# Kernel tuning notes

Hardware: AMD Instinct MI355X
Metric: run time of the kernel (lower is better)

## Reference

```python
import jax, jax.numpy as jnp
import numpy as np

B, S, HID = 4, 1024, 1024
NH, HD = 16, 64  # num heads, head dim


def setup_inputs() -> dict:
    key = jax.random.key(0)
    ks = jax.random.split(key, 8)
    scale = 0.02
    return {
        "hidden_states": jax.random.normal(ks[0], (B, S, HID), dtype=jnp.float32),
        "attention_mask": jnp.ones((B, 1, 1, S), dtype=jnp.float32),
        "Wq": jax.random.normal(ks[1], (HID, HID), dtype=jnp.float32) * scale,
        "bq": jnp.zeros((HID,), dtype=jnp.float32),
        "Wk": jax.random.normal(ks[2], (HID, HID), dtype=jnp.float32) * scale,
        "bk": jnp.zeros((HID,), dtype=jnp.float32),
        "Wv": jax.random.normal(ks[3], (HID, HID), dtype=jnp.float32) * scale,
        "bv": jnp.zeros((HID,), dtype=jnp.float32),
    }


def reference(hidden_states, attention_mask, Wq, bq, Wk, bk, Wv, bv):
    # Linear projections: torch nn.Linear computes x @ W.T + b
    q = hidden_states @ Wq.T + bq  # [B,S,HID]
    k = hidden_states @ Wk.T + bk
    v = hidden_states @ Wv.T + bv

    def split_heads(x):
        return x.reshape(B, S, NH, HD).transpose(0, 2, 1, 3)  # [B,NH,S,HD]

    q, k, v = split_heads(q), split_heads(k), split_heads(v)

    scores = jnp.einsum("bhqd,bhkd->bhqk", q, k) / jnp.sqrt(jnp.float32(HD))
    # faithful to original: scores - (2 - mask) * 1e6
    scores = scores - (2.0 - attention_mask) * 1.0e6
    probs = jax.nn.softmax(scores, axis=-1)
    # dropout: eval mode -> identity
    ctx = jnp.einsum("bhqk,bhkd->bhqd", probs, v)  # [B,NH,S,HD]
    ctx = ctx.transpose(0, 2, 1, 3).reshape(B, S, HID)
    return ctx
```

## Files before the change

### kernel.cpp

```cpp
#include <hip/hip_runtime.h>
#include <math.h>

#define B_ 4
#define S_ 1024
#define HID_ 1024
#define NH_ 16
#define HD_ 64
#define NTOK (B_ * S_)

typedef __attribute__((ext_vector_type(4))) float f32x4;
typedef __attribute__((ext_vector_type(8))) short bf16x8;

__device__ __forceinline__ unsigned short f2bf(float f) {
    union { float f; unsigned int u; } v; v.f = f;
    unsigned int r = v.u + 0x7fffu + ((v.u >> 16) & 1u);
    return (unsigned short)(r >> 16);
}
__device__ __forceinline__ float bf2f(unsigned short u) {
    return __uint_as_float((unsigned int)u << 16);
}

__device__ __forceinline__ void load_lds16(const void* g, void* l) {
    __builtin_amdgcn_global_load_lds(
        (const __attribute__((address_space(1))) unsigned int*)(uintptr_t)g,
        (__attribute__((address_space(3))) unsigned int*)(uintptr_t)l,
        16, 0, 0);
}

__global__ __launch_bounds__(256) void cvt_all(
    const float* __restrict__ x, const float* __restrict__ wq,
    const float* __restrict__ wk, const float* __restrict__ wv,
    unsigned short* __restrict__ xb, unsigned short* __restrict__ wqb,
    unsigned short* __restrict__ wkb, unsigned short* __restrict__ wvb)
{
    const int which = blockIdx.y;
    const float* src = which == 0 ? x : which == 1 ? wq : which == 2 ? wk : wv;
    unsigned short* dst = which == 0 ? xb : which == 1 ? wqb : which == 2 ? wkb : wvb;
    const int n4 = (which == 0) ? (NTOK * HID_ / 4) : (HID_ * HID_ / 4);
    int i = blockIdx.x * 256 + threadIdx.x;
    if (i < n4) {
        float4 f = ((const float4*)src)[i];
        ushort4 o = make_ushort4(f2bf(f.x), f2bf(f.y), f2bf(f.z), f2bf(f.w));
        ((ushort4*)dst)[i] = o;
    }
}

__global__ __launch_bounds__(256) void qkv_gemm_mfma(
    const unsigned short* __restrict__ xb,
    const unsigned short* __restrict__ Wqb, const float* __restrict__ bq,
    const unsigned short* __restrict__ Wkb, const float* __restrict__ bk,
    const unsigned short* __restrict__ Wvb, const float* __restrict__ bv,
    unsigned short* __restrict__ qout, unsigned short* __restrict__ kout,
    unsigned short* __restrict__ vtout)
{
    const int which = blockIdx.z;
    const unsigned short* __restrict__ W = which == 0 ? Wqb : which == 1 ? Wkb : Wvb;
    const float* __restrict__ bias       = which == 0 ? bq  : which == 1 ? bk  : bv;

    __shared__ unsigned short As[128 * 64];
    __shared__ unsigned short Bs[128 * 64];

    const int t    = threadIdx.x;
    const int lane = t & 63;
    const int w    = t >> 6;
    const int wr   = w >> 1;
    const int wc   = w & 1;
    const int g    = lane >> 4;
    const int lrow = lane & 15;

    const int bm = blockIdx.x;
    const int bn = blockIdx.y;

    const unsigned short* __restrict__ Arow = (which == 2) ? W  : xb;
    const unsigned short* __restrict__ Brow = (which == 2) ? xb : W;
    const int am0 = (which == 2) ? bn * 128 : bm * 128;
    const int bn0 = (which == 2) ? bm * 128 : bn * 128;

    const int srow = t >> 3;
    const int sc   = ((t & 7) ^ ((t >> 3) & 7)) << 3;
    const unsigned short* gA = Arow + (size_t)(am0 + srow) * HID_ + sc;
    const unsigned short* gB = Brow + (size_t)(bn0 + srow) * HID_ + sc;

    const f32x4 zero = {0.f, 0.f, 0.f, 0.f};
    f32x4 acc[4][4];
    #pragma unroll
    for (int i = 0; i < 4; ++i)
        #pragma unroll
        for (int j = 0; j < 4; ++j) acc[i][j] = zero;

    for (int k0 = 0; k0 < HID_; k0 += 64) {
        __syncthreads();
        #pragma unroll
        for (int i = 0; i < 4; ++i) {
            load_lds16(gA + (size_t)(i * 32) * HID_ + k0, (char*)As + i * 4096 + t * 16);
            load_lds16(gB + (size_t)(i * 32) * HID_ + k0, (char*)Bs + i * 4096 + t * 16);
        }
        __syncthreads();

        #pragma unroll
        for (int ks = 0; ks < 2; ++ks) {
            bf16x8 af[4], bf[4];
            #pragma unroll
            for (int i = 0; i < 4; ++i) {
                const int row = wr * 64 + i * 16 + lrow;
                af[i] = *(const bf16x8*)&As[row * 64 + (((ks * 4 + g) ^ (row & 7)) << 3)];
            }
            #pragma unroll
            for (int j = 0; j < 4; ++j) {
                const int row = wc * 64 + j * 16 + lrow;
                bf[j] = *(const bf16x8*)&Bs[row * 64 + (((ks * 4 + g) ^ (row & 7)) << 3)];
            }
            #pragma unroll
            for (int i = 0; i < 4; ++i)
                #pragma unroll
                for (int j = 0; j < 4; ++j)
                    acc[i][j] = __builtin_amdgcn_mfma_f32_16x16x32_bf16(
                        af[i], bf[j], acc[i][j], 0, 0, 0);
        }
    }

    const int col   = lane & 15;
    const int rbase = (lane >> 4) << 2;
    if (which == 2) {
        #pragma unroll
        for (int i = 0; i < 4; ++i) {
            #pragma unroll
            for (int r = 0; r < 4; ++r) {
                const int feat = bn * 128 + wr * 64 + i * 16 + rbase + r;
                const int h = feat >> 6, d = feat & 63;
                const float bias_v = bias[feat];
                #pragma unroll
                for (int j = 0; j < 4; ++j) {
                    const int tok = bm * 128 + wc * 64 + j * 16 + col;
                    const int b = tok >> 10, s = tok & 1023;
                    vtout[((size_t)((b << 4) + h) << 16) + ((size_t)d << 10) + s] =
                        f2bf(acc[i][j][r] + bias_v);
                }
            }
        }
    } else {
        #pragma unroll
        for (int j = 0; j < 4; ++j) {
            const int feat = bn * 128 + wc * 64 + j * 16 + col;
            const int h = feat >> 6, d = feat & 63;
            const float bias_v = bias[feat];
            #pragma unroll
            for (int i = 0; i < 4; ++i) {
                const int tok0 = bm * 128 + wr * 64 + i * 16 + rbase;
                #pragma unroll
                for (int r = 0; r < 4; ++r) {
                    const int tok = tok0 + r;
                    const int b = tok >> 10, s = tok & 1023;
                    const size_t off = ((size_t)((b << 4) + h) << 16) + ((size_t)s << 6) + d;
                    const float val = acc[i][j][r] + bias_v;
                    if (which == 0) qout[off] = f2bf(val);
                    else            kout[off] = f2bf(val);
                }
            }
        }
    }
}

__global__ __launch_bounds__(256) void attn_mfma(
    const unsigned short* __restrict__ Q, const unsigned short* __restrict__ K,
    const unsigned short* __restrict__ Vt, const float* __restrict__ mask,
    float* __restrict__ out)
{
    __shared__ unsigned short Qs[64 * 64];
    __shared__ unsigned short Ks[64 * 64];
    __shared__ unsigned short Vts[64 * 64];
    __shared__ unsigned short Ps[4][16 * 72];
    __shared__ float Ls[4][16];
    __shared__ float Ms[64];

    const int t    = threadIdx.x;
    const int lane = t & 63;
    const int w    = t >> 6;
    const int g    = lane >> 4;
    const int ln   = lane & 15;

    const int bh = blockIdx.x;
    const int b  = bh >> 4;
    const int h  = bh & 15;
    const int q0 = blockIdx.y << 6;

    const unsigned short* __restrict__ qg = Q  + ((size_t)bh << 16);
    const unsigned short* __restrict__ kg = K  + ((size_t)bh << 16);
    const unsigned short* __restrict__ vg = Vt + ((size_t)bh << 16);

    #pragma unroll
    for (int i = 0; i < 2; ++i) {
        const int G   = i * 256 + t;
        const int row = G >> 3;
        const int c   = (G & 7) ^ (row & 7);
        load_lds16(qg + (size_t)(q0 + row) * 64 + c * 8, (char*)Qs + i * 4096 + t * 16);
    }

    const f32x4 zero = {0.f, 0.f, 0.f, 0.f};
    f32x4 O[4];
    #pragma unroll
    for (int j = 0; j < 4; ++j) O[j] = zero;
    float lacc = 0.f;

    const int qrow = w * 16 + ln;

    for (int kt = 0; kt < 16; ++kt) {
        const int kt0 = kt << 6;
        __syncthreads();
        #pragma unroll
        for (int i = 0; i < 2; ++i) {
            const int G   = i * 256 + t;
            const int row = G >> 3;
            const int c   = (G & 7) ^ (row & 7);
            load_lds16(kg + (size_t)(kt0 + row) * 64 + c * 8, (char*)Ks  + i * 4096 + t * 16);
            load_lds16(vg + (size_t)row * 1024 + kt0 + c * 8, (char*)Vts + i * 4096 + t * 16);
        }
        if (t < 64) Ms[t] = mask[(b << 10) + kt0 + t];
        __syncthreads();

        f32x4 sacc[4];
        #pragma unroll
        for (int j = 0; j < 4; ++j) sacc[j] = zero;
        #pragma unroll
        for (int ks = 0; ks < 2; ++ks) {
            bf16x8 qf = *(const bf16x8*)&Qs[qrow * 64 + (((ks * 4 + g) ^ (qrow & 7)) << 3)];
            bf16x8 kf[4];
            #pragma unroll
            for (int j = 0; j < 4; ++j) {
                const int krow = j * 16 + ln;
                kf[j] = *(const bf16x8*)&Ks[krow * 64 + (((ks * 4 + g) ^ (krow & 7)) << 3)];
            }
            #pragma unroll
            for (int j = 0; j < 4; ++j)
                sacc[j] = __builtin_amdgcn_mfma_f32_16x16x32_bf16(
                    kf[j], qf, sacc[j], 0, 0, 0);
        }

        #pragma unroll
        for (int j = 0; j < 4; ++j) {
            unsigned short pb[4];
            #pragma unroll
            for (int r = 0; r < 4; ++r) {
                const int key = j * 16 + g * 4 + r;
                const float sv = sacc[j][r] * 0.125f - (2.0f - Ms[key]) * 1.0e6f;
                pb[r] = f2bf(__expf(sv + 1.0e6f));
                lacc += bf2f(pb[r]);
            }
            uint2 pk;
            pk.x = (unsigned int)pb[0] | ((unsigned int)pb[1] << 16);
            pk.y = (unsigned int)pb[2] | ((unsigned int)pb[3] << 16);
            *(uint2*)&Ps[w][ln * 72 + j * 16 + (g << 2)] = pk;
        }
        asm volatile("s_waitcnt lgkmcnt(0)" ::: "memory");

        #pragma unroll
        for (int ks = 0; ks < 2; ++ks) {
            bf16x8 pf = *(const bf16x8*)&Ps[w][ln * 72 + ks * 32 + (g << 3)];
            bf16x8 vf[4];
            #pragma unroll
            for (int j = 0; j < 4; ++j) {
                const int vrow = j * 16 + ln;
                vf[j] = *(const bf16x8*)&Vts[vrow * 64 + (((ks * 4 + g) ^ (vrow & 7)) << 3)];
            }
            #pragma unroll
            for (int j = 0; j < 4; ++j)
                O[j] = __builtin_amdgcn_mfma_f32_16x16x32_bf16(
                    pf, vf[j], O[j], 0, 0, 0);
        }
    }

    float rs = lacc;
    rs += __shfl_xor(rs, 16);
    rs += __shfl_xor(rs, 32);
    if (lane < 16) Ls[w][ln] = rs;
    asm volatile("s_waitcnt lgkmcnt(0)" ::: "memory");
    #pragma unroll
    for (int r = 0; r < 4; ++r) {
        const float inv = 1.0f / Ls[w][(g << 2) + r];
        const int q = q0 + w * 16 + (g << 2) + r;
        const size_t base = (((size_t)(b << 10) + q) << 10) + (h << 6);
        #pragma unroll
        for (int j = 0; j < 4; ++j)
            out[base + j * 16 + ln] = O[j][r] * inv;
    }
}

extern "C" void kernel_launch(void* const* d_in, const int* in_sizes, int n_in,
                              void* d_out, int out_size, void* d_ws, size_t ws_size,
                              hipStream_t stream) {
    const float* hs   = (const float*)d_in[0];
    const float* mask = (const float*)d_in[1];
    const float* Wq   = (const float*)d_in[2];
    const float* bq   = (const float*)d_in[3];
    const float* Wk   = (const float*)d_in[4];
    const float* bk   = (const float*)d_in[5];
    const float* Wv   = (const float*)d_in[6];
    const float* bv   = (const float*)d_in[7];
    float* out = (float*)d_out;

    char* ws = (char*)d_ws;
    unsigned short* xb  = (unsigned short*)(ws);
    unsigned short* wqb = (unsigned short*)(ws + ((size_t)8  << 20));
    unsigned short* wkb = (unsigned short*)(ws + ((size_t)10 << 20));
    unsigned short* wvb = (unsigned short*)(ws + ((size_t)12 << 20));
    unsigned short* qb  = (unsigned short*)(ws + ((size_t)14 << 20));
    unsigned short* kb  = (unsigned short*)(ws + ((size_t)22 << 20));
    unsigned short* vtb = (unsigned short*)(ws + ((size_t)30 << 20));

    cvt_all<<<dim3(4096, 4), 256, 0, stream>>>(hs, Wq, Wk, Wv, xb, wqb, wkb, wvb);
    qkv_gemm_mfma<<<dim3(NTOK / 128, HID_ / 128, 3), 256, 0, stream>>>(
        xb, wqb, bq, wkb, bk, wvb, bv, qb, kb, vtb);
    attn_mfma<<<dim3(B_ * NH_, S_ / 64), 256, 0, stream>>>(qb, kb, vtb, mask, out);
}
```

Baseline: 162.7 us.

## Double-buffer K/V/mask tiles in attention kernel to overlap loads with compute

Makes the K, V^T and mask shared-memory tiles double-buffered and preloads the first tile before the loop. Each iteration now issues the asynchronous global-to-LDS loads for the next key tile right after the barrier, then computes on the current tile. This drops one barrier per iteration and is meant to hide global load latency behind the MFMA and softmax work. The cost is roughly double the LDS for K/V, which can lower occupancy. The overlap also depends on the compiler not inserting conservative waits on the async loads.

```diff
diff --git a/kernel.cpp b/kernel.cpp
--- a/kernel.cpp
+++ b/kernel.cpp
@@ -167,11 +167,11 @@
     float* __restrict__ out)
 {
     __shared__ unsigned short Qs[64 * 64];
-    __shared__ unsigned short Ks[64 * 64];
-    __shared__ unsigned short Vts[64 * 64];
+    __shared__ unsigned short Ks[2][64 * 64];
+    __shared__ unsigned short Vts[2][64 * 64];
     __shared__ unsigned short Ps[4][16 * 72];
+    __shared__ float Ms[2][64];
     __shared__ float Ls[4][16];
-    __shared__ float Ms[64];
 
     const int t    = threadIdx.x;
     const int lane = t & 63;
@@ -188,13 +188,21 @@
     const unsigned short* __restrict__ kg = K  + ((size_t)bh << 16);
     const unsigned short* __restrict__ vg = Vt + ((size_t)bh << 16);
 
+    const int srow0 = t >> 3;
+    const int sc0   = ((t & 7) ^ ((t >> 3) & 7));
+
     #pragma unroll
     for (int i = 0; i < 2; ++i) {
-        const int G   = i * 256 + t;
-        const int row = G >> 3;
-        const int c   = (G & 7) ^ (row & 7);
-        load_lds16(qg + (size_t)(q0 + row) * 64 + c * 8, (char*)Qs + i * 4096 + t * 16);
-    }
+        const int row = i * 32 + srow0;
+        load_lds16(qg + (size_t)(q0 + row) * 64 + sc0 * 8, (char*)Qs + i * 4096 + t * 16);
+    }
+    #pragma unroll
+    for (int i = 0; i < 2; ++i) {
+        const int row = i * 32 + srow0;
+        load_lds16(kg + (size_t)row * 64 + sc0 * 8,  (char*)Ks[0]  + i * 4096 + t * 16);
+        load_lds16(vg + (size_t)row * 1024 + sc0 * 8,(char*)Vts[0] + i * 4096 + t * 16);
+    }
+    if (t < 64) Ms[0][t] = mask[(b << 10) + t];
 
     const f32x4 zero = {0.f, 0.f, 0.f, 0.f};
     f32x4 O[4];
@@ -205,19 +213,24 @@
     const int qrow = w * 16 + ln;
 
     for (int kt = 0; kt < 16; ++kt) {
+        const int cur = kt & 1;
+        __syncthreads();
+
+        float mval = 0.f;
+        if (kt < 15) {
+            const int nt0 = (kt + 1) << 6;
+            if (t < 64) mval = mask[(b << 10) + nt0 + t];
+            #pragma unroll
+            for (int i = 0; i < 2; ++i) {
+                const int row = i * 32 + srow0;
+                load_lds16(kg + (size_t)(nt0 + row) * 64 + sc0 * 8,
+                           (char*)Ks[cur ^ 1]  + i * 4096 + t * 16);
+                load_lds16(vg + (size_t)row * 1024 + nt0 + sc0 * 8,
+                           (char*)Vts[cur ^ 1] + i * 4096 + t * 16);
+            }
+        }
+
         const int kt0 = kt << 6;
-        __syncthreads();
-        #pragma unroll
-        for (int i = 0; i < 2; ++i) {
-            const int G   = i * 256 + t;
-            const int row = G >> 3;
-            const int c   = (G & 7) ^ (row & 7);
-            load_lds16(kg + (size_t)(kt0 + row) * 64 + c * 8, (char*)Ks  + i * 4096 + t * 16);
-            load_lds16(vg + (size_t)row * 1024 + kt0 + c * 8, (char*)Vts + i * 4096 + t * 16);
-        }
-        if (t < 64) Ms[t] = mask[(b << 10) + kt0 + t];
-        __syncthreads();
-
         f32x4 sacc[4];
         #pragma unroll
         for (int j = 0; j < 4; ++j) sacc[j] = zero;
@@ -228,13 +241,14 @@
             #pragma unroll
             for (int j = 0; j < 4; ++j) {
                 const int krow = j * 16 + ln;
-                kf[j] = *(const bf16x8*)&Ks[krow * 64 + (((ks * 4 + g) ^ (krow & 7)) << 3)];
+                kf[j] = *(const bf16x8*)&Ks[cur][krow * 64 + (((ks * 4 + g) ^ (krow & 7)) << 3)];
             }
             #pragma unroll
             for (int j = 0; j < 4; ++j)
                 sacc[j] = __builtin_amdgcn_mfma_f32_16x16x32_bf16(
                     kf[j], qf, sacc[j], 0, 0, 0);
         }
+        (void)kt0;
 
         #pragma unroll
         for (int j = 0; j < 4; ++j) {
@@ -242,7 +256,7 @@
             #pragma unroll
             for (int r = 0; r < 4; ++r) {
                 const int key = j * 16 + g * 4 + r;
-                const float sv = sacc[j][r] * 0.125f - (2.0f - Ms[key]) * 1.0e6f;
+                const float sv = sacc[j][r] * 0.125f - (2.0f - Ms[cur][key]) * 1.0e6f;
                 pb[r] = f2bf(__expf(sv + 1.0e6f));
                 lacc += bf2f(pb[r]);
             }
@@ -260,13 +274,15 @@
             #pragma unroll
             for (int j = 0; j < 4; ++j) {
                 const int vrow = j * 16 + ln;
-                vf[j] = *(const bf16x8*)&Vts[vrow * 64 + (((ks * 4 + g) ^ (vrow & 7)) << 3)];
+                vf[j] = *(const bf16x8*)&Vts[cur][vrow * 64 + (((ks * 4 + g) ^ (vrow & 7)) << 3)];
             }
             #pragma unroll
             for (int j = 0; j < 4; ++j)
                 O[j] = __builtin_amdgcn_mfma_f32_16x16x32_bf16(
                     pf, vf[j], O[j], 0, 0, 0);
         }
+
+        if (kt < 15 && t < 64) Ms[cur ^ 1][t] = mval;
     }
 
     float rs = lacc;
```

New measurement: 166.6 us. 2.4% more time.
